# Kernel optimization log

Measured on AMD Instinct MI355X. Metric: run time of the kernel, lower is better.

## Reference

```python
import jax, jax.numpy as jnp
import numpy as np

B, T, D = 4, 2048, 1024
H, DH = 16, 64

def setup_inputs() -> dict:
    key = jax.random.key(0)
    k1, k2, k3 = jax.random.split(key, 3)
    x = jax.random.normal(k1, (B, T, D), dtype=jnp.float32)
    ln_gamma = jnp.ones((D,), dtype=jnp.float32)
    ln_beta = jnp.zeros((D,), dtype=jnp.float32)
    W_qkv = jax.random.normal(k2, (3 * D, D), dtype=jnp.float32) * (1.0 / np.sqrt(D))
    W_o = jax.random.normal(k3, (D, D), dtype=jnp.float32) * (1.0 / np.sqrt(D))
    return {"x": x, "ln_gamma": ln_gamma, "ln_beta": ln_beta, "W_qkv": W_qkv, "W_o": W_o}

def reference(x, ln_gamma, ln_beta, W_qkv, W_o):
    b, t, d = x.shape
    scale = 1.0 / np.sqrt(DH)
    # pre-LN in fp32 (eps=1e-5, elementwise affine)
    xf = x.astype(jnp.float32)
    mu = jnp.mean(xf, axis=-1, keepdims=True)
    var = jnp.mean(jnp.square(xf - mu), axis=-1, keepdims=True)
    xn = (xf - mu) * jax.lax.rsqrt(var + 1e-5) * ln_gamma + ln_beta
    xn = xn.astype(x.dtype)
    # fused QKV projection (torch Linear: y = x @ W^T), view as (B,T,H,3*DH)
    qkv = jnp.einsum('btd,ed->bte', xn, W_qkv).reshape(b, t, H, 3 * DH)
    Q, K, V = jnp.split(qkv, 3, axis=-1)  # each (B,T,H,DH)
    # scores (B,H,T,T), causal mask, softmax
    scores = jnp.einsum('bqhd,bkhd->bhqk', Q, K) * scale
    causal = jnp.tril(jnp.ones((t, t), dtype=bool))
    scores = jnp.where(causal, scores, -jnp.inf)
    A = jax.nn.softmax(scores, axis=-1)
    ctx = jnp.einsum('bhqk,bkhd->bqhd', A, V).reshape(b, t, d)
    return jnp.einsum('btd,ed->bte', ctx, W_o)
```

## Files before the change

### kernel.cpp

```cpp
#include <hip/hip_runtime.h>


typedef __attribute__((ext_vector_type(8))) short bf8v;
typedef __attribute__((ext_vector_type(4))) float f4v;

#define Tt  2048
#define Dd  1024
#define Hh  16
#define DHh 64

#if __has_builtin(__builtin_amdgcn_exp2f)
#define EXP2(x) __builtin_amdgcn_exp2f(x)
#else
#define EXP2(x) __expf((x) * 0.69314718056f)
#endif

__device__ __forceinline__ ushort f2bf(float f) {
  union { float f; unsigned v; } c; c.f = f;
  unsigned r = c.v + 0x7fffu + ((c.v >> 16) & 1u);
  return (ushort)(r >> 16);
}
__device__ __forceinline__ ushort f2bf_rn(float f) {
  union { float f; unsigned v; } c; c.f = f;
  return (ushort)((c.v + 0x8000u) >> 16);
}
__device__ __forceinline__ f4v zero4() { f4v z; z[0]=z[1]=z[2]=z[3]=0.f; return z; }

__device__ __forceinline__ void gl_lds16(const ushort* g, ushort* l) {
  __builtin_amdgcn_global_load_lds(
      (const __attribute__((address_space(1))) unsigned*)g,
      (__attribute__((address_space(3))) unsigned*)l, 16, 0, 0);
}

__global__ __launch_bounds__(256)
void cvt_k(const float* __restrict__ src, ushort* __restrict__ dst) {
  const int i = blockIdx.x * 256 + threadIdx.x;
  const float4 v = ((const float4*)src)[i];
  ushort4 o;
  o.x = f2bf(v.x); o.y = f2bf(v.y); o.z = f2bf(v.z); o.w = f2bf(v.w);
  ((ushort4*)dst)[i] = o;
}

__global__ __launch_bounds__(256)
void ln_k(const float* __restrict__ x, const float* __restrict__ g,
          const float* __restrict__ bta, ushort* __restrict__ xn) {
  const int row = blockIdx.x, tid = threadIdx.x;
  const float4 v = ((const float4*)(x + row * Dd))[tid];
  float s  = v.x + v.y + v.z + v.w;
  float sq = v.x*v.x + v.y*v.y + v.z*v.z + v.w*v.w;
  #pragma unroll
  for (int off = 32; off; off >>= 1) {
    s  += __shfl_down(s,  off, 64);
    sq += __shfl_down(sq, off, 64);
  }
  __shared__ float red[8];
  const int w = tid >> 6, l = tid & 63;
  if (l == 0) { red[w] = s; red[w + 4] = sq; }
  __syncthreads();
  s  = red[0] + red[1] + red[2] + red[3];
  sq = red[4] + red[5] + red[6] + red[7];
  const float mu  = s * (1.0f / Dd);
  const float var = sq * (1.0f / Dd) - mu * mu;
  const float rs  = rsqrtf(var + 1e-5f);
  const float4 gv = ((const float4*)g)[tid];
  const float4 bv = ((const float4*)bta)[tid];
  ushort4 o;
  o.x = f2bf((v.x - mu) * rs * gv.x + bv.x);
  o.y = f2bf((v.y - mu) * rs * gv.y + bv.y);
  o.z = f2bf((v.z - mu) * rs * gv.z + bv.z);
  o.w = f2bf((v.w - mu) * rs * gv.w + bv.w);
  ((ushort4*)(xn + row * Dd))[tid] = o;
}

template<int MODE>
__global__ __launch_bounds__(256)
void gemm128(const ushort* __restrict__ A, const ushort* __restrict__ Bt,
             void* __restrict__ O0v, ushort* __restrict__ O1, ushort* __restrict__ O2,
             int Kd, int nbm) {
  __shared__ ushort As[2][128 * 64], Bs[2][128 * 64];
  const int tid = threadIdx.x;
  const int l = tid & 63, w = tid >> 6, fr = l & 15, fq = l >> 4;
  const int wm = w & 1, wn = w >> 1;
  const int bm = blockIdx.x % nbm, bn = blockIdx.x / nbm;
  const int gr8 = l >> 3, gc8s = ((l & 7) ^ gr8) * 8;
  const int sw = fr & 7;
  const int cA = (fq ^ sw) * 8, cB = ((4 + fq) ^ sw) * 8;
  const int NIT = Kd >> 6;

  f4v acc[4][4];
  #pragma unroll
  for (int m = 0; m < 4; m++)
    #pragma unroll
    for (int n = 0; n < 4; n++) acc[m][n] = zero4();

  auto stage = [&](int it, int bi) {
    const int k0 = it * 64;
    #pragma unroll
    for (int i = 0; i < 4; i++) {
      const int row = w * 32 + i * 8;
      gl_lds16(A  + (bm * 128 + row + gr8) * Kd + k0 + gc8s, &As[bi][row * 64]);
      gl_lds16(Bt + (bn * 128 + row + gr8) * Kd + k0 + gc8s, &Bs[bi][row * 64]);
    }
  };

  stage(0, 0);
  for (int it = 0; it < NIT; ++it) {
    __syncthreads();
    if (it + 1 < NIT) stage(it + 1, (it + 1) & 1);
    const ushort* Ab = As[it & 1];
    const ushort* Bb = Bs[it & 1];
    #pragma unroll
    for (int kk = 0; kk < 2; kk++) {
      const int cs = kk ? cB : cA;
      bf8v af[4], bf[4];
      #pragma unroll
      for (int m = 0; m < 4; m++)
        af[m] = *(const bf8v*)&Ab[(wm * 64 + m * 16 + fr) * 64 + cs];
      #pragma unroll
      for (int n = 0; n < 4; n++)
        bf[n] = *(const bf8v*)&Bb[(wn * 64 + n * 16 + fr) * 64 + cs];
      #pragma unroll
      for (int m = 0; m < 4; m++)
        #pragma unroll
        for (int n = 0; n < 4; n++)
          acc[m][n] = __builtin_amdgcn_mfma_f32_16x16x32_bf16(af[m], bf[n], acc[m][n], 0, 0, 0);
    }
  }

  #pragma unroll
  for (int m = 0; m < 4; m++) {
    const int grow = bm * 128 + wm * 64 + m * 16 + fq * 4;
    #pragma unroll
    for (int n = 0; n < 4; n++) {
      const int e = bn * 128 + wn * 64 + n * 16 + fr;
      #pragma unroll
      for (int r = 0; r < 4; r++) {
        const int row = grow + r;
        if (MODE == 0) {
          const int h = e / 192, inner = e % 192;
          const int sel = inner >> 6, dh = inner & 63;
          const int bb = row >> 11, t = row & 2047;
          float v = acc[m][n][r];
          if (sel == 0) v *= 0.18033688f;
          ushort* dst = (sel == 0) ? (ushort*)O0v : (sel == 1) ? O1 : O2;
          dst[((bb * Hh + h) * Tt + t) * DHh + dh] = f2bf(v);
        } else {
          ((float*)O0v)[row * Dd + e] = acc[m][n][r];
        }
      }
    }
  }
}

__global__ __launch_bounds__(256)
void vtr_k(const ushort* __restrict__ Vb, ushort* __restrict__ Vtg) {
  __shared__ ushort tile[64 * 72];
  const int tid = threadIdx.x;
  const int tt = blockIdx.x & 31;
  const int hb = blockIdx.x >> 5;
  const int base = hb * Tt * DHh;
  const int srow = tid >> 3, soff = (tid & 7) * 8;
  #pragma unroll
  for (int i = 0; i < 2; i++) {
    const int t = srow + i * 32;
    const uint4 vv = *(const uint4*)(Vb + base + (tt * 64 + t) * DHh + soff);
    const ushort* e = (const ushort*)&vv;
    #pragma unroll
    for (int j = 0; j < 8; j++) tile[(soff + j) * 72 + t] = e[j];
  }
  __syncthreads();
  #pragma unroll
  for (int i = 0; i < 2; i++) {
    const int dh = srow + i * 32;
    *(uint4*)(Vtg + base + dh * Tt + tt * 64 + soff) = *(const uint4*)&tile[dh * 72 + soff];
  }
}

__global__ __launch_bounds__(256)
void attn_k(const ushort* __restrict__ Qb, const ushort* __restrict__ Kb,
            const ushort* __restrict__ Vtg, ushort* __restrict__ ctx) {
  __shared__ ushort QP[128 * 64];
  __shared__ ushort Ks[2][64 * 64], Vt[2][64 * 64];
  const int tid = threadIdx.x;
  const int l = tid & 63, w = tid >> 6, fr = l & 15, fq = l >> 4;
  const int bid = blockIdx.x;
  const int hb = (bid & 7) * 8 + (bid >> 6);
  const int u  = (bid >> 3) & 7;
  const int h  = hb & 15, b = hb >> 4;
  const int headbase = hb * Tt * DHh;
  const int gr8 = l >> 3, gc8s = ((l & 7) ^ gr8) * 8;
  const int sw = fr & 7;
  const int cA = (fq ^ sw) * 8, cB = ((4 + fq) ^ sw) * 8;

  auto stageKV = [&](int kt, int bi) {
    #pragma unroll
    for (int i = 0; i < 2; i++) {
      const int row = w * 16 + i * 8;
      gl_lds16(Kb  + headbase + (kt * 64 + row + gr8) * DHh + gc8s, &Ks[bi][row * 64]);
      gl_lds16(Vtg + headbase + (row + gr8) * Tt + kt * 64 + gc8s, &Vt[bi][row * 64]);
    }
  };

  for (int half = 0; half < 2; ++half) {
    const int qt = half ? (15 - u) : u;
    const int qrow0w = qt * 128 + w * 32;

    if (half) __syncthreads();

    #pragma unroll
    for (int i = 0; i < 4; i++) {
      const int row = w * 32 + i * 8;
      gl_lds16(Qb + headbase + (qt * 128 + row + gr8) * DHh + gc8s, &QP[row * 64]);
    }
    stageKV(0, 0);
    __syncthreads();

    bf8v aq[2][2];
    #pragma unroll
    for (int m = 0; m < 2; m++) {
      aq[m][0] = *(const bf8v*)&QP[(w * 32 + m * 16 + fr) * 64 + cA];
      aq[m][1] = *(const bf8v*)&QP[(w * 32 + m * 16 + fr) * 64 + cB];
    }
    __asm__ __volatile__("" ::: "memory");

    f4v o[2][4];
    #pragma unroll
    for (int m = 0; m < 2; m++)
      #pragma unroll
      for (int n = 0; n < 4; n++) o[m][n] = zero4();
    float lst[2][4] = {{0.f,0.f,0.f,0.f},{0.f,0.f,0.f,0.f}};

    const int ktmax = 2 * qt + 1;
    for (int kt = 0; kt <= ktmax; ++kt) {
      if (kt) __syncthreads();
      if (kt < ktmax) stageKV(kt + 1, (kt + 1) & 1);
      const ushort* K_ = Ks[kt & 1];
      const ushort* V_ = Vt[kt & 1];

      if (kt * 64 <= qrow0w + 31) {
        f4v sc[2][4];
        #pragma unroll
        for (int m = 0; m < 2; m++)
          #pragma unroll
          for (int n = 0; n < 4; n++) sc[m][n] = zero4();
        #pragma unroll
        for (int nt = 0; nt < 4; nt++) {
          const bf8v b0 = *(const bf8v*)&K_[(nt * 16 + fr) * 64 + cA];
          const bf8v b1 = *(const bf8v*)&K_[(nt * 16 + fr) * 64 + cB];
          #pragma unroll
          for (int m = 0; m < 2; m++) {
            sc[m][nt] = __builtin_amdgcn_mfma_f32_16x16x32_bf16(aq[m][0], b0, sc[m][nt], 0, 0, 0);
            sc[m][nt] = __builtin_amdgcn_mfma_f32_16x16x32_bf16(aq[m][1], b1, sc[m][nt], 0, 0, 0);
          }
        }

        if (kt * 64 + 63 > qrow0w) {
          #pragma unroll
          for (int m = 0; m < 2; m++) {
            const int q0 = qrow0w + m * 16 + fq * 4;
            #pragma unroll
            for (int nt = 0; nt < 4; nt++) {
              const int kc = kt * 64 + nt * 16 + fr;
              #pragma unroll
              for (int r = 0; r < 4; r++)
                if (kc > q0 + r) sc[m][nt][r] = -1e30f;
            }
          }
        }

        #pragma unroll
        for (int m = 0; m < 2; m++)
          #pragma unroll
          for (int r = 0; r < 4; r++) {
            const int prow = w * 32 + m * 16 + fq * 4 + r;
            const int psw = prow & 7;
            const int pb = prow * 64 + (fr & 7);
            const int c8 = fr >> 3;
            const float p0 = EXP2(sc[m][0][r]), p1 = EXP2(sc[m][1][r]);
            const float p2 = EXP2(sc[m][2][r]), p3 = EXP2(sc[m][3][r]);
            QP[pb + ((c8    ) ^ psw) * 8] = f2bf_rn(p0);
            QP[pb + ((c8 + 2) ^ psw) * 8] = f2bf_rn(p1);
            QP[pb + ((c8 + 4) ^ psw) * 8] = f2bf_rn(p2);
            QP[pb + ((c8 + 6) ^ psw) * 8] = f2bf_rn(p3);
            lst[m][r] += (p0 + p1) + (p2 + p3);
          }

        __asm__ __volatile__("" ::: "memory");

        #pragma unroll
        for (int s = 0; s < 2; s++) {
          const int cs = s ? cB : cA;
          const bf8v ap0 = *(const bf8v*)&QP[(w * 32 + fr) * 64 + cs];
          const bf8v ap1 = *(const bf8v*)&QP[(w * 32 + 16 + fr) * 64 + cs];
          #pragma unroll
          for (int nt = 0; nt < 4; nt++) {
            const bf8v bv2 = *(const bf8v*)&V_[(nt * 16 + fr) * 64 + cs];
            o[0][nt] = __builtin_amdgcn_mfma_f32_16x16x32_bf16(ap0, bv2, o[0][nt], 0, 0, 0);
            o[1][nt] = __builtin_amdgcn_mfma_f32_16x16x32_bf16(ap1, bv2, o[1][nt], 0, 0, 0);
          }
        }
      }
    }

    #pragma unroll
    for (int m = 0; m < 2; m++)
      #pragma unroll
      for (int r = 0; r < 4; r++) {
        float t = lst[m][r];
        t += __shfl_xor(t, 1, 64); t += __shfl_xor(t, 2, 64);
        t += __shfl_xor(t, 4, 64); t += __shfl_xor(t, 8, 64);
        const float inv = 1.0f / t;
        const int rowg = b * Tt + qt * 128 + w * 32 + m * 16 + fq * 4 + r;
        #pragma unroll
        for (int nt = 0; nt < 4; nt++)
          ctx[rowg * Dd + h * DHh + nt * 16 + fr] = f2bf(o[m][nt][r] * inv);
      }
  }
}

extern "C" void kernel_launch(void* const* d_in, const int* in_sizes, int n_in,
                              void* d_out, int out_size, void* d_ws, size_t ws_size,
                              hipStream_t stream) {
  const float* x    = (const float*)d_in[0];
  const float* g    = (const float*)d_in[1];
  const float* bta  = (const float*)d_in[2];
  const float* wqkv = (const float*)d_in[3];
  const float* wo   = (const float*)d_in[4];

  const int NROW = 4 * Tt;
  const int NQ   = 4 * Hh * Tt * DHh;
  ushort* xn   = (ushort*)d_ws;
  ushort* Qb   = xn + NROW * Dd;
  ushort* Kb   = Qb + NQ;
  ushort* Vb   = Kb + NQ;
  ushort* ctx  = Vb + NQ;
  ushort* wqkb = ctx + NROW * Dd;
  ushort* wob  = wqkb + 3 * Dd * Dd;
  ushort* VbT  = xn;

  cvt_k<<<3 * Dd * Dd / 1024, 256, 0, stream>>>(wqkv, wqkb);
  cvt_k<<<Dd * Dd / 1024, 256, 0, stream>>>(wo, wob);
  ln_k<<<NROW, 256, 0, stream>>>(x, g, bta, xn);
  gemm128<0><<<64 * 24, 256, 0, stream>>>(xn, wqkb, Qb, Kb, Vb, Dd, 64);
  vtr_k<<<4 * Hh * (Tt / 64), 256, 0, stream>>>(Vb, VbT);
  attn_k<<<4 * Hh * (Tt / 128) / 2, 256, 0, stream>>>(Qb, Kb, VbT, ctx);
  gemm128<1><<<64 * 8, 256, 0, stream>>>(ctx, wob, (void*)d_out, nullptr, nullptr, Dd, 64);
}
```

Measured before the change: 257.5 us.

## Compute transposed S tile so P stores vectorize and row sums stay per-lane

Swaps the MFMA operands so each lane holds four consecutive key columns of one query row. P can then be written to LDS as a single 8-byte ushort4 store per tile instead of four scalar stores, and the row-sum accumulator shrinks to one value per m. The final normalization uses two shuffles plus a lane gather instead of four-step reductions per row. It also raises wave priority around the MFMA blocks via s_setprio, which changes scheduling and may starve other waves.

Result: no change. 254.4 us (-1.2%).

```diff
diff --git a/kernel.cpp b/kernel.cpp
--- a/kernel.cpp
+++ b/kernel.cpp
@@ -228,7 +228,7 @@
     for (int m = 0; m < 2; m++)
       #pragma unroll
       for (int n = 0; n < 4; n++) o[m][n] = zero4();
-    float lst[2][4] = {{0.f,0.f,0.f,0.f},{0.f,0.f,0.f,0.f}};
+    float lsum[2] = {0.f, 0.f};
 
     const int ktmax = 2 * qt + 1;
     for (int kt = 0; kt <= ktmax; ++kt) {
@@ -238,55 +238,60 @@
       const ushort* V_ = Vt[kt & 1];
 
       if (kt * 64 <= qrow0w + 31) {
-        f4v sc[2][4];
+        f4v scT[2][4];
         #pragma unroll
         for (int m = 0; m < 2; m++)
           #pragma unroll
-          for (int n = 0; n < 4; n++) sc[m][n] = zero4();
+          for (int n = 0; n < 4; n++) scT[m][n] = zero4();
+        __builtin_amdgcn_s_setprio(1);
         #pragma unroll
         for (int nt = 0; nt < 4; nt++) {
-          const bf8v b0 = *(const bf8v*)&K_[(nt * 16 + fr) * 64 + cA];
-          const bf8v b1 = *(const bf8v*)&K_[(nt * 16 + fr) * 64 + cB];
+          const bf8v k0 = *(const bf8v*)&K_[(nt * 16 + fr) * 64 + cA];
+          const bf8v k1 = *(const bf8v*)&K_[(nt * 16 + fr) * 64 + cB];
           #pragma unroll
           for (int m = 0; m < 2; m++) {
-            sc[m][nt] = __builtin_amdgcn_mfma_f32_16x16x32_bf16(aq[m][0], b0, sc[m][nt], 0, 0, 0);
-            sc[m][nt] = __builtin_amdgcn_mfma_f32_16x16x32_bf16(aq[m][1], b1, sc[m][nt], 0, 0, 0);
+            scT[m][nt] = __builtin_amdgcn_mfma_f32_16x16x32_bf16(k0, aq[m][0], scT[m][nt], 0, 0, 0);
+            scT[m][nt] = __builtin_amdgcn_mfma_f32_16x16x32_bf16(k1, aq[m][1], scT[m][nt], 0, 0, 0);
           }
         }
+        __builtin_amdgcn_s_setprio(0);
 
         if (kt * 64 + 63 > qrow0w) {
           #pragma unroll
           for (int m = 0; m < 2; m++) {
-            const int q0 = qrow0w + m * 16 + fq * 4;
+            const int q0 = qrow0w + m * 16 + fr;
             #pragma unroll
             for (int nt = 0; nt < 4; nt++) {
-              const int kc = kt * 64 + nt * 16 + fr;
+              const int kc0 = kt * 64 + nt * 16 + fq * 4;
               #pragma unroll
               for (int r = 0; r < 4; r++)
-                if (kc > q0 + r) sc[m][nt][r] = -1e30f;
+                if (kc0 + r > q0) scT[m][nt][r] = -1e30f;
             }
           }
         }
 
         #pragma unroll
-        for (int m = 0; m < 2; m++)
-          #pragma unroll
-          for (int r = 0; r < 4; r++) {
-            const int prow = w * 32 + m * 16 + fq * 4 + r;
-            const int psw = prow & 7;
-            const int pb = prow * 64 + (fr & 7);
-            const int c8 = fr >> 3;
-            const float p0 = EXP2(sc[m][0][r]), p1 = EXP2(sc[m][1][r]);
-            const float p2 = EXP2(sc[m][2][r]), p3 = EXP2(sc[m][3][r]);
-            QP[pb + ((c8    ) ^ psw) * 8] = f2bf_rn(p0);
-            QP[pb + ((c8 + 2) ^ psw) * 8] = f2bf_rn(p1);
-            QP[pb + ((c8 + 4) ^ psw) * 8] = f2bf_rn(p2);
-            QP[pb + ((c8 + 6) ^ psw) * 8] = f2bf_rn(p3);
-            lst[m][r] += (p0 + p1) + (p2 + p3);
+        for (int m = 0; m < 2; m++) {
+          const int prow = w * 32 + m * 16 + fr;
+          const int psw = fr & 7;
+          ushort* base = &QP[prow * 64];
+          #pragma unroll
+          for (int nt = 0; nt < 4; nt++) {
+            const int g = 2 * nt + (fq >> 1);
+            const int off = ((g ^ psw) << 3) + ((fq & 1) << 2);
+            const float p0 = EXP2(scT[m][nt][0]), p1 = EXP2(scT[m][nt][1]);
+            const float p2 = EXP2(scT[m][nt][2]), p3 = EXP2(scT[m][nt][3]);
+            ushort4 pk;
+            pk.x = f2bf_rn(p0); pk.y = f2bf_rn(p1);
+            pk.z = f2bf_rn(p2); pk.w = f2bf_rn(p3);
+            *(ushort4*)(base + off) = pk;
+            lsum[m] += (p0 + p1) + (p2 + p3);
           }
+        }
 
         __asm__ __volatile__("" ::: "memory");
 
+        __builtin_amdgcn_s_setprio(1);
         #pragma unroll
         for (int s = 0; s < 2; s++) {
           const int cs = s ? cB : cA;
@@ -299,21 +304,27 @@
             o[1][nt] = __builtin_amdgcn_mfma_f32_16x16x32_bf16(ap1, bv2, o[1][nt], 0, 0, 0);
           }
         }
+        __builtin_amdgcn_s_setprio(0);
       }
     }
 
+    float inv[2];
+    #pragma unroll
+    for (int m = 0; m < 2; m++) {
+      float t = lsum[m];
+      t += __shfl_xor(t, 16, 64);
+      t += __shfl_xor(t, 32, 64);
+      inv[m] = 1.0f / t;
+    }
     #pragma unroll
     for (int m = 0; m < 2; m++)
       #pragma unroll
       for (int r = 0; r < 4; r++) {
-        float t = lst[m][r];
-        t += __shfl_xor(t, 1, 64); t += __shfl_xor(t, 2, 64);
-        t += __shfl_xor(t, 4, 64); t += __shfl_xor(t, 8, 64);
-        const float inv = 1.0f / t;
+        const float iv = __shfl(inv[m], 20 * fq + r, 64);
         const int rowg = b * Tt + qt * 128 + w * 32 + m * 16 + fq * 4 + r;
         #pragma unroll
         for (int nt = 0; nt < 4; nt++)
-          ctx[rowg * Dd + h * DHh + nt * 16 + fr] = f2bf(o[m][nt][r] * inv);
+          ctx[rowg * Dd + h * DHh + nt * 16 + fr] = f2bf(o[m][nt][r] * iv);
       }
   }
 }
```
